# Kernel tuning notes

Hardware: AMD Instinct MI355X
Metric: run time of the kernel (lower is better)

## Reference

```python
import jax, jax.numpy as jnp
import numpy as np

B, T, D, H = 2, 2048, 1024, 16
HD = D // H  # head_dim = 64


def apply_rope(x, cos, sin):
    # x: [B, H, T, HD]; cos/sin: [1, 1, T, HD//2]
    x1, x2 = x[..., ::2], x[..., 1::2]
    y1 = x1 * cos - x2 * sin
    y2 = x1 * sin + x2 * cos
    # interleave back: [..., HD//2, 2] -> [..., HD]
    return jnp.stack([y1, y2], axis=-1).reshape(x.shape)


def setup_inputs() -> dict:
    key = jax.random.key(0)
    ks = jax.random.split(key, 11)
    s = 0.02
    return {
        "x": jax.random.normal(ks[0], (B, T, D), jnp.float32),
        "cos": jax.random.normal(ks[1], (1, 1, T, HD // 2), jnp.float32),
        "sin": jax.random.normal(ks[2], (1, 1, T, HD // 2), jnp.float32),
        "Wq": jax.random.normal(ks[3], (D, D), jnp.float32) * s,
        "bq": jax.random.normal(ks[4], (D,), jnp.float32) * s,
        "Wk": jax.random.normal(ks[5], (D, D), jnp.float32) * s,
        "bk": jax.random.normal(ks[6], (D,), jnp.float32) * s,
        "Wv": jax.random.normal(ks[7], (D, D), jnp.float32) * s,
        "bv": jax.random.normal(ks[8], (D,), jnp.float32) * s,
        "Wo": jax.random.normal(ks[9], (D, D), jnp.float32) * s,
        "bo": jax.random.normal(ks[10], (D,), jnp.float32) * s,
    }


def reference(x, cos, sin, Wq, bq, Wk, bk, Wv, bv, Wo, bo):
    b, t, d = x.shape
    # projections (nn.Linear: x @ W.T + b)
    q = (x @ Wq.T + bq).reshape(b, t, H, HD).transpose(0, 2, 1, 3)
    k = (x @ Wk.T + bk).reshape(b, t, H, HD).transpose(0, 2, 1, 3)
    v = (x @ Wv.T + bv).reshape(b, t, H, HD).transpose(0, 2, 1, 3)
    q = apply_rope(q, cos, sin)
    k = apply_rope(k, cos, sin)
    scores = jnp.einsum("bhqd,bhkd->bhqk", q, k) / jnp.sqrt(jnp.asarray(HD, x.dtype))
    # causal mask: query i attends to keys j <= i
    causal = jnp.tril(jnp.ones((t, t), dtype=bool))
    scores = jnp.where(causal, scores, jnp.asarray(-jnp.inf, x.dtype))
    weights = jax.nn.softmax(scores, axis=-1)
    out = jnp.einsum("bhqk,bhkd->bhqd", weights, v)
    out = out.transpose(0, 2, 1, 3).reshape(b, t, d)
    return out @ Wo.T + bo
```

## Files before the change

kernel.cpp:

```cpp
#include <hip/hip_runtime.h>
#include <hip/hip_bf16.h>
#include <cstdint>
#include <cstddef>

typedef __attribute__((ext_vector_type(8))) short bf16x8;
typedef __attribute__((ext_vector_type(4))) float f32x4;
typedef __attribute__((ext_vector_type(16))) float f32x16;

#define SCALE2 0.180336880111112f
#define VSTRIDE 2080

__device__ __forceinline__ unsigned short f2bf(float f) {
    unsigned u = __builtin_bit_cast(unsigned, f);
    unsigned r = (u + 0x7FFFu + ((u >> 16) & 1u)) >> 16;
    return (unsigned short)r;
}

__device__ __forceinline__ void gload16(const unsigned short* g, unsigned short* l) {
    __builtin_amdgcn_global_load_lds(
        (const __attribute__((address_space(1))) unsigned int*)(g),
        (__attribute__((address_space(3))) unsigned int*)(l), 16, 0, 0);
}

__global__ void cvt_all(const float* __restrict__ x,
                        const float* __restrict__ wq, const float* __restrict__ wk,
                        const float* __restrict__ wv, const float* __restrict__ wo,
                        unsigned short* __restrict__ xb,
                        unsigned short* __restrict__ wqb, unsigned short* __restrict__ wkb,
                        unsigned short* __restrict__ wvb, unsigned short* __restrict__ wob)
{
    const int y = blockIdx.y;
    const float* src; unsigned short* dst; int n;
    switch (y) {
        case 0: src = x;  dst = xb;  n = 4194304; break;
        case 1: src = wq; dst = wqb; n = 1048576; break;
        case 2: src = wk; dst = wkb; n = 1048576; break;
        case 3: src = wv; dst = wvb; n = 1048576; break;
        default: src = wo; dst = wob; n = 1048576; break;
    }
    const int i = (blockIdx.x * 256 + threadIdx.x) * 4;
    if (i < n) {
        float4 v = *(const float4*)(src + i);
        ushort4 o;
        o.x = f2bf(v.x); o.y = f2bf(v.y); o.z = f2bf(v.z); o.w = f2bf(v.w);
        *(ushort4*)(dst + i) = o;
    }
}

__global__ __launch_bounds__(256) void gemm_qkv(
    const unsigned short* __restrict__ xb,
    const unsigned short* __restrict__ wqb,
    const unsigned short* __restrict__ wkb,
    const unsigned short* __restrict__ wvb,
    const float* __restrict__ bq, const float* __restrict__ bk, const float* __restrict__ bv,
    const float* __restrict__ cosT, const float* __restrict__ sinT,
    unsigned short* __restrict__ Qb, unsigned short* __restrict__ Kb, unsigned short* __restrict__ Vtg)
{
    const int z = blockIdx.z;
    const unsigned short* wb = (z == 0) ? wqb : ((z == 1) ? wkb : wvb);
    const float* bias = (z == 0) ? bq : ((z == 1) ? bk : bv);
    unsigned short* dst = (z == 0) ? Qb : Kb;

    __shared__ __align__(16) unsigned short Al[128 * 32];
    __shared__ __align__(16) unsigned short Bl[128 * 32];
    __shared__ __align__(16) unsigned short Ct[128 * 136];

    const int tid = threadIdx.x;
    const int lane = tid & 63;
    const int w = tid >> 6;
    const int wr = w >> 1, wc = w & 1;
    const int lr = lane & 15, lg = lane >> 4;
    const int m0 = blockIdx.y * 128;
    const int n0 = blockIdx.x * 128;
    const int srow = tid >> 2, sseg = tid & 3;
    const int wbase = tid & 192;

    f32x4 acc[4][4] = {};

    for (int k0 = 0; k0 < 1024; k0 += 32) {
        __syncthreads();
#pragma unroll
        for (int p = 0; p < 2; ++p) {
            const int row = srow + p * 64;
            gload16(xb + (size_t)(m0 + row) * 1024 + k0 + sseg * 8, Al + (p * 256 + wbase) * 8);
            gload16(wb + (size_t)(n0 + row) * 1024 + k0 + sseg * 8, Bl + (p * 256 + wbase) * 8);
        }
        __syncthreads();
        bf16x8 af[4], bfr[4];
#pragma unroll
        for (int mt = 0; mt < 4; ++mt)
            af[mt] = *(const bf16x8*)(Al + (wr * 64 + mt * 16 + lr) * 32 + lg * 8);
#pragma unroll
        for (int nt = 0; nt < 4; ++nt)
            bfr[nt] = *(const bf16x8*)(Bl + (wc * 64 + nt * 16 + lr) * 32 + lg * 8);
#pragma unroll
        for (int mt = 0; mt < 4; ++mt)
#pragma unroll
            for (int nt = 0; nt < 4; ++nt)
                acc[mt][nt] = __builtin_amdgcn_mfma_f32_16x16x32_bf16(af[mt], bfr[nt], acc[mt][nt], 0, 0, 0);
    }

#pragma unroll
    for (int mt = 0; mt < 4; ++mt) {
#pragma unroll
        for (int nt = 0; nt < 4; ++nt) {
            const int coln = wc * 64 + nt * 16 + lr;
            const int col = n0 + coln;
            const float bcol = bias[col];
            const int hd = col & 63;
#pragma unroll
            for (int r = 0; r < 4; ++r) {
                const int rowm = wr * 64 + mt * 16 + lg * 4 + r;
                float v = acc[mt][nt][r] + bcol;
                if (z < 2) {
                    float part = __shfl_xor(v, 1);
                    const int tt = (m0 + rowm) & 2047;
                    const int i = hd >> 1;
                    const float cc = cosT[tt * 32 + i], ss = sinT[tt * 32 + i];
                    v = (hd & 1) ? (part * ss + v * cc) : (v * cc - part * ss);
                    if (z == 0) v *= SCALE2;
                    Ct[rowm * 136 + coln] = f2bf(v);
                } else {
                    Ct[coln * 136 + rowm] = f2bf(v);
                }
            }
        }
    }
    __syncthreads();
    if (z < 2) {
#pragma unroll
        for (int p = 0; p < 8; ++p) {
            const int u = p * 256 + tid;
            const int row = u >> 4, seg = u & 15;
            bf16x8 vv = *(const bf16x8*)(Ct + row * 136 + seg * 8);
            const int mrow = m0 + row;
            const int tt = mrow & 2047, bb = mrow >> 11;
            const int col = n0 + seg * 8;
            const int h = col >> 6, hd = col & 63;
            *(bf16x8*)(dst + ((size_t)(bb * 16 + h) * 2048 + tt) * 64 + hd) = vv;
        }
    } else {
        const int bb = m0 >> 11;
#pragma unroll
        for (int p = 0; p < 8; ++p) {
            const int u = p * 256 + tid;
            const int vrow = u >> 4, seg = u & 15;
            bf16x8 vv = *(const bf16x8*)(Ct + vrow * 136 + seg * 8);
            const int col = n0 + vrow;
            const int h = col >> 6, hd = col & 63;
            const int tt = (m0 + seg * 8) & 2047;
            *(bf16x8*)(Vtg + ((size_t)(bb * 16 + h) * 64 + hd) * VSTRIDE + tt) = vv;
        }
    }
}

__global__ __launch_bounds__(256, 2) void attn_fwd(
    const unsigned short* __restrict__ Qb, const unsigned short* __restrict__ Kb,
    const unsigned short* __restrict__ Vtg, unsigned short* __restrict__ attnb)
{
    __shared__ __align__(16) unsigned short Kl[2][32 * 64];
    __shared__ __align__(16) unsigned short Vl[2][64 * 32];
    __shared__ __align__(16) float Om[2][32][64];
    __shared__ float Ms[2][64];

    const int tid = threadIdx.x, lane = tid & 63, w = tid >> 6;
    const int l31 = lane & 31, lh = lane >> 5;
    const int bid = blockIdx.x;
    const int bh = bid & 31;
    const int pi = bid >> 5;
    const int half = w >> 1;
    const int slice = w & 1;
    const int cH = 63 - pi;
    const int c = half ? pi : cH;
    const size_t base = (size_t)bh * 131072;
    const int myq = c * 32 + l31;

    const unsigned short* Kg = Kb + base;
    const unsigned short* Vg = Vtg + (size_t)bh * (64 * VSTRIDE);

    bf16x8 qf[4];
#pragma unroll
    for (int s = 0; s < 4; ++s)
        qf[s] = *(const bf16x8*)(Qb + base + (size_t)myq * 64 + s * 16 + lh * 8);

    f32x16 o0 = {}, o1 = {};
    float sm = 0.f;

    const int krow = tid >> 3, kseg = (tid & 7) ^ (krow & 7);
    const int vrow = tid >> 2, vseg = (tid & 3) ^ (vrow & 3);
    const int ldst = (tid & ~63) * 8;

#define STAGE(T, B)                                                                  \
    {                                                                                \
        gload16(Kg + (size_t)((T) * 32 + krow) * 64 + kseg * 8, &Kl[B][ldst]);       \
        gload16(Vg + (size_t)vrow * VSTRIDE + (T) * 32 + vseg * 8, &Vl[B][ldst]);    \
    }

    STAGE(0, 0);
    for (int t = 0; t <= cH; ++t) {
        asm volatile("s_waitcnt vmcnt(0)" ::: "memory");
        __syncthreads();
        if (t + 1 <= cH) STAGE(t + 1, (t + 1) & 1);
        if (t <= c && (t & 1) == slice) {
            const unsigned short* Kc = Kl[t & 1];
            const unsigned short* Vc = Vl[t & 1];
            const int kvb = t * 32;

            bf16x8 kf0 = *(const bf16x8*)(Kc + l31 * 64 + (((0 * 2 + lh)) ^ (l31 & 7)) * 8);
            bf16x8 kf1 = *(const bf16x8*)(Kc + l31 * 64 + (((1 * 2 + lh)) ^ (l31 & 7)) * 8);
            bf16x8 kf2 = *(const bf16x8*)(Kc + l31 * 64 + (((2 * 2 + lh)) ^ (l31 & 7)) * 8);
            bf16x8 kf3 = *(const bf16x8*)(Kc + l31 * 64 + (((3 * 2 + lh)) ^ (l31 & 7)) * 8);

            f32x16 st = {};
            st = __builtin_amdgcn_mfma_f32_32x32x16_bf16(kf0, qf[0], st, 0, 0, 0);
            st = __builtin_amdgcn_mfma_f32_32x32x16_bf16(kf1, qf[1], st, 0, 0, 0);
            st = __builtin_amdgcn_mfma_f32_32x32x16_bf16(kf2, qf[2], st, 0, 0, 0);
            st = __builtin_amdgcn_mfma_f32_32x32x16_bf16(kf3, qf[3], st, 0, 0, 0);

            if (t == c) {
#pragma unroll
                for (int r = 0; r < 16; ++r) {
                    const int kv = kvb + (r & 3) + 8 * (r >> 2) + 4 * lh;
                    st[r] = (kv <= myq) ? st[r] : -1e30f;
                }
            }
#pragma unroll
            for (int r = 0; r < 16; ++r) st[r] = exp2f(st[r]);
            {
                float a0 = st[0] + st[1], a1 = st[2] + st[3];
                float a2 = st[4] + st[5], a3 = st[6] + st[7];
                float a4 = st[8] + st[9], a5 = st[10] + st[11];
                float a6 = st[12] + st[13], a7 = st[14] + st[15];
                sm += ((a0 + a1) + (a2 + a3)) + ((a4 + a5) + (a6 + a7));
            }

            unsigned pw0, pw1, pw2, pw3, pw4, pw5, pw6, pw7;
            {
                unsigned a0, a1, b0, b1;
                asm("v_cvt_pk_bf16_f32 %0, %1, %2" : "=v"(a0) : "v"(st[0]), "v"(st[1]));
                asm("v_cvt_pk_bf16_f32 %0, %1, %2" : "=v"(a1) : "v"(st[2]), "v"(st[3]));
                asm("v_cvt_pk_bf16_f32 %0, %1, %2" : "=v"(b0) : "v"(st[4]), "v"(st[5]));
                asm("v_cvt_pk_bf16_f32 %0, %1, %2" : "=v"(b1) : "v"(st[6]), "v"(st[7]));
                asm("v_permlane32_swap_b32 %0, %1" : "+v"(a0), "+v"(b0));
                asm("v_permlane32_swap_b32 %0, %1" : "+v"(a1), "+v"(b1));
                pw0 = a0; pw1 = a1; pw2 = b0; pw3 = b1;
            }
            {
                unsigned a0, a1, b0, b1;
                asm("v_cvt_pk_bf16_f32 %0, %1, %2" : "=v"(a0) : "v"(st[8]), "v"(st[9]));
                asm("v_cvt_pk_bf16_f32 %0, %1, %2" : "=v"(a1) : "v"(st[10]), "v"(st[11]));
                asm("v_cvt_pk_bf16_f32 %0, %1, %2" : "=v"(b0) : "v"(st[12]), "v"(st[13]));
                asm("v_cvt_pk_bf16_f32 %0, %1, %2" : "=v"(b1) : "v"(st[14]), "v"(st[15]));
                asm("v_permlane32_swap_b32 %0, %1" : "+v"(a0), "+v"(b0));
                asm("v_permlane32_swap_b32 %0, %1" : "+v"(a1), "+v"(b1));
                pw4 = a0; pw5 = a1; pw6 = b0; pw7 = b1;
            }

            const int vsw = l31 & 3;
            bf16x8 vf00 = *(const bf16x8*)(Vc + l31 * 32 + ((lh) ^ vsw) * 8);
            bf16x8 vf01 = *(const bf16x8*)(Vc + l31 * 32 + ((2 + lh) ^ vsw) * 8);
            bf16x8 vf10 = *(const bf16x8*)(Vc + (32 + l31) * 32 + ((lh) ^ vsw) * 8);
            bf16x8 vf11 = *(const bf16x8*)(Vc + (32 + l31) * 32 + ((2 + lh) ^ vsw) * 8);

            uint4 h0 = make_uint4(pw0, pw1, pw2, pw3);
            uint4 h1 = make_uint4(pw4, pw5, pw6, pw7);
            bf16x8 pf0 = __builtin_bit_cast(bf16x8, h0);
            bf16x8 pf1 = __builtin_bit_cast(bf16x8, h1);
            o0 = __builtin_amdgcn_mfma_f32_32x32x16_bf16(vf00, pf0, o0, 0, 0, 0);
            o1 = __builtin_amdgcn_mfma_f32_32x32x16_bf16(vf10, pf0, o1, 0, 0, 0);
            o0 = __builtin_amdgcn_mfma_f32_32x32x16_bf16(vf01, pf1, o0, 0, 0, 0);
            o1 = __builtin_amdgcn_mfma_f32_32x32x16_bf16(vf11, pf1, o1, 0, 0, 0);
        }
    }

    sm += __shfl_xor(sm, 32);

    __syncthreads();
    if (slice == 1) {
#pragma unroll
        for (int i = 0; i < 16; ++i) Om[half][i][lane] = o0[i];
#pragma unroll
        for (int i = 0; i < 16; ++i) Om[half][16 + i][lane] = o1[i];
        Ms[half][lane] = sm;
    }
    __syncthreads();
    if (slice == 0) {
        const float s = sm + Ms[half][lane];
        const float inv = 1.f / s;
        const int b = bh >> 4, h = bh & 15;
        unsigned short* obase = attnb + ((size_t)(b * 2048 + myq)) * 1024 + h * 64;
#pragma unroll
        for (int g = 0; g < 4; ++g) {
            ushort4 u;
            u.x = f2bf((o0[g * 4 + 0] + Om[half][g * 4 + 0][lane]) * inv);
            u.y = f2bf((o0[g * 4 + 1] + Om[half][g * 4 + 1][lane]) * inv);
            u.z = f2bf((o0[g * 4 + 2] + Om[half][g * 4 + 2][lane]) * inv);
            u.w = f2bf((o0[g * 4 + 3] + Om[half][g * 4 + 3][lane]) * inv);
            *(ushort4*)(obase + g * 8 + lh * 4) = u;
            ushort4 v;
            v.x = f2bf((o1[g * 4 + 0] + Om[half][16 + g * 4 + 0][lane]) * inv);
            v.y = f2bf((o1[g * 4 + 1] + Om[half][16 + g * 4 + 1][lane]) * inv);
            v.z = f2bf((o1[g * 4 + 2] + Om[half][16 + g * 4 + 2][lane]) * inv);
            v.w = f2bf((o1[g * 4 + 3] + Om[half][16 + g * 4 + 3][lane]) * inv);
            *(ushort4*)(obase + 32 + g * 8 + lh * 4) = v;
        }
    }
#undef STAGE
}

__global__ __launch_bounds__(256) void gemm_out(
    const unsigned short* __restrict__ ab,
    const unsigned short* __restrict__ wob,
    const float* __restrict__ bo,
    float* __restrict__ out)
{
    __shared__ __align__(16) unsigned short Al[128 * 32];
    __shared__ __align__(16) unsigned short Bl[64 * 32];

    const int tid = threadIdx.x;
    const int lane = tid & 63;
    const int w = tid >> 6;
    const int lr = lane & 15, lg = lane >> 4;
    const int m0 = blockIdx.y * 128;
    const int n0 = blockIdx.x * 64;

    f32x4 acc[2][4] = {};

    for (int k0 = 0; k0 < 1024; k0 += 32) {
        __syncthreads();
#pragma unroll
        for (int p = 0; p < 2; ++p) {
            const int u = p * 256 + tid;
            const int row = u >> 2, seg = u & 3;
            gload16(ab + (size_t)(m0 + row) * 1024 + k0 + seg * 8, Al + (u & ~63) * 8);
        }
        {
            const int u = tid;
            const int row = u >> 2, seg = u & 3;
            gload16(wob + (size_t)(n0 + row) * 1024 + k0 + seg * 8, Bl + (u & ~63) * 8);
        }
        __syncthreads();
        bf16x8 af[2], bfr[4];
#pragma unroll
        for (int mt = 0; mt < 2; ++mt)
            af[mt] = *(const bf16x8*)(Al + (w * 32 + mt * 16 + lr) * 32 + lg * 8);
#pragma unroll
        for (int nt = 0; nt < 4; ++nt)
            bfr[nt] = *(const bf16x8*)(Bl + (nt * 16 + lr) * 32 + lg * 8);
#pragma unroll
        for (int mt = 0; mt < 2; ++mt)
#pragma unroll
            for (int nt = 0; nt < 4; ++nt)
                acc[mt][nt] = __builtin_amdgcn_mfma_f32_16x16x32_bf16(af[mt], bfr[nt], acc[mt][nt], 0, 0, 0);
    }

#pragma unroll
    for (int mt = 0; mt < 2; ++mt) {
#pragma unroll
        for (int nt = 0; nt < 4; ++nt) {
            const int col = n0 + nt * 16 + lr;
            const float bcol = bo[col];
#pragma unroll
            for (int r = 0; r < 4; ++r) {
                const int mrow = m0 + w * 32 + mt * 16 + lg * 4 + r;
                out[(size_t)mrow * 1024 + col] = acc[mt][nt][r] + bcol;
            }
        }
    }
}

extern "C" void kernel_launch(void* const* d_in, const int* in_sizes, int n_in,
                              void* d_out, int out_size, void* d_ws, size_t ws_size,
                              hipStream_t stream) {
    const float* x    = (const float*)d_in[0];
    const float* cosT = (const float*)d_in[1];
    const float* sinT = (const float*)d_in[2];
    const float* Wq   = (const float*)d_in[3];
    const float* bq   = (const float*)d_in[4];
    const float* Wk   = (const float*)d_in[5];
    const float* bk   = (const float*)d_in[6];
    const float* Wv   = (const float*)d_in[7];
    const float* bv   = (const float*)d_in[8];
    const float* Wo   = (const float*)d_in[9];
    const float* bo   = (const float*)d_in[10];
    float* out = (float*)d_out;

    char* ws = (char*)d_ws;
    unsigned short* xb    = (unsigned short*)(ws + 0);
    unsigned short* attnb = (unsigned short*)(ws + 0);
    unsigned short* wob   = (unsigned short*)(ws + 8388608);
    unsigned short* wqb   = (unsigned short*)(ws + 10485760);
    unsigned short* wkb   = (unsigned short*)(ws + 12582912);
    unsigned short* wvb   = (unsigned short*)(ws + 14680064);
    unsigned short* Qb    = (unsigned short*)(ws + 16777216);
    unsigned short* Kb    = (unsigned short*)(ws + 25165824);
    unsigned short* Vtg   = (unsigned short*)(ws + 33554432);

    cvt_all<<<dim3(4096, 5), 256, 0, stream>>>(x, Wq, Wk, Wv, Wo, xb, wqb, wkb, wvb, wob);
    gemm_qkv<<<dim3(8, 32, 3), 256, 0, stream>>>(xb, wqb, wkb, wvb, bq, bk, bv,
                                                 cosT, sinT, Qb, Kb, Vtg);
    attn_fwd<<<dim3(1024), 256, 0, stream>>>(Qb, Kb, Vtg, attnb);
    gemm_out<<<dim3(16, 32), 256, 0, stream>>>(attnb, wob, bo, out);
}
```

Measured before the change: 131.6 us.

## Triple-buffer attention K/V loads and remap GEMM blocks for XCD-local L2 reuse

The attention kernel moves from double to triple buffering of K/V tiles in one shared byte buffer. It prefetches two tiles ahead and waits with vmcnt(2), so global loads overlap compute longer. The shared region is reused for the final cross-warp reduction. Both GEMMs switch to a 1D grid whose block index maps tiles so that blocks on the same XCD (bid&7) share A/B row and column panels, aiming at better L2 locality. The trade-off is more LDS per attention block, which may lower occupancy, and more index arithmetic.

```diff
diff --git a/kernel.cpp b/kernel.cpp
--- a/kernel.cpp
+++ b/kernel.cpp
@@ -56,7 +56,15 @@
     const float* __restrict__ cosT, const float* __restrict__ sinT,
     unsigned short* __restrict__ Qb, unsigned short* __restrict__ Kb, unsigned short* __restrict__ Vtg)
 {
-    const int z = blockIdx.z;
+    const int bid = blockIdx.x;
+    const int xcd = bid & 7;
+    const int s = bid >> 3;
+    const int i4 = xcd >> 1, k2 = xcd & 1;
+    const int z = s >> 5;
+    const int tt = s & 31;
+    const int m0 = (i4 * 8 + (tt >> 2)) * 128;
+    const int n0 = (k2 * 4 + (tt & 3)) * 128;
+
     const unsigned short* wb = (z == 0) ? wqb : ((z == 1) ? wkb : wvb);
     const float* bias = (z == 0) ? bq : ((z == 1) ? bk : bv);
     unsigned short* dst = (z == 0) ? Qb : Kb;
@@ -70,8 +78,6 @@
     const int w = tid >> 6;
     const int wr = w >> 1, wc = w & 1;
     const int lr = lane & 15, lg = lane >> 4;
-    const int m0 = blockIdx.y * 128;
-    const int n0 = blockIdx.x * 128;
     const int srow = tid >> 2, sseg = tid & 3;
     const int wbase = tid & 192;
 
@@ -114,9 +120,9 @@
                 float v = acc[mt][nt][r] + bcol;
                 if (z < 2) {
                     float part = __shfl_xor(v, 1);
-                    const int tt = (m0 + rowm) & 2047;
+                    const int ttm = (m0 + rowm) & 2047;
                     const int i = hd >> 1;
-                    const float cc = cosT[tt * 32 + i], ss = sinT[tt * 32 + i];
+                    const float cc = cosT[ttm * 32 + i], ss = sinT[ttm * 32 + i];
                     v = (hd & 1) ? (part * ss + v * cc) : (v * cc - part * ss);
                     if (z == 0) v *= SCALE2;
                     Ct[rowm * 136 + coln] = f2bf(v);
@@ -134,10 +140,10 @@
             const int row = u >> 4, seg = u & 15;
             bf16x8 vv = *(const bf16x8*)(Ct + row * 136 + seg * 8);
             const int mrow = m0 + row;
-            const int tt = mrow & 2047, bb = mrow >> 11;
+            const int ttm = mrow & 2047, bb = mrow >> 11;
             const int col = n0 + seg * 8;
             const int h = col >> 6, hd = col & 63;
-            *(bf16x8*)(dst + ((size_t)(bb * 16 + h) * 2048 + tt) * 64 + hd) = vv;
+            *(bf16x8*)(dst + ((size_t)(bb * 16 + h) * 2048 + ttm) * 64 + hd) = vv;
         }
     } else {
         const int bb = m0 >> 11;
@@ -148,8 +154,8 @@
             bf16x8 vv = *(const bf16x8*)(Ct + vrow * 136 + seg * 8);
             const int col = n0 + vrow;
             const int h = col >> 6, hd = col & 63;
-            const int tt = (m0 + seg * 8) & 2047;
-            *(bf16x8*)(Vtg + ((size_t)(bb * 16 + h) * 64 + hd) * VSTRIDE + tt) = vv;
+            const int ttm = (m0 + seg * 8) & 2047;
+            *(bf16x8*)(Vtg + ((size_t)(bb * 16 + h) * 64 + hd) * VSTRIDE + ttm) = vv;
         }
     }
 }
@@ -158,10 +164,7 @@
     const unsigned short* __restrict__ Qb, const unsigned short* __restrict__ Kb,
     const unsigned short* __restrict__ Vtg, unsigned short* __restrict__ attnb)
 {
-    __shared__ __align__(16) unsigned short Kl[2][32 * 64];
-    __shared__ __align__(16) unsigned short Vl[2][64 * 32];
-    __shared__ __align__(16) float Om[2][32][64];
-    __shared__ float Ms[2][64];
+    __shared__ __align__(16) unsigned char smem[25088];
 
     const int tid = threadIdx.x, lane = tid & 63, w = tid >> 6;
     const int l31 = lane & 31, lh = lane >> 5;
@@ -190,26 +193,37 @@
     const int vrow = tid >> 2, vseg = (tid & 3) ^ (vrow & 3);
     const int ldst = (tid & ~63) * 8;
 
-#define STAGE(T, B)                                                                  \
-    {                                                                                \
-        gload16(Kg + (size_t)((T) * 32 + krow) * 64 + kseg * 8, &Kl[B][ldst]);       \
-        gload16(Vg + (size_t)vrow * VSTRIDE + (T) * 32 + vseg * 8, &Vl[B][ldst]);    \
+#define STAGE(T, B)                                                                   \
+    {                                                                                 \
+        unsigned short* kb_ = (unsigned short*)(smem + (B) * 8192);                   \
+        unsigned short* vb_ = (unsigned short*)(smem + (B) * 8192 + 4096);            \
+        gload16(Kg + (size_t)((T) * 32 + krow) * 64 + kseg * 8, kb_ + ldst);          \
+        gload16(Vg + (size_t)vrow * VSTRIDE + (T) * 32 + vseg * 8, vb_ + ldst);       \
     }
 
     STAGE(0, 0);
+    STAGE(1, 1);
+    int bsel = 0;
     for (int t = 0; t <= cH; ++t) {
-        asm volatile("s_waitcnt vmcnt(0)" ::: "memory");
+        if (t < cH) asm volatile("s_waitcnt vmcnt(2)" ::: "memory");
+        else        asm volatile("s_waitcnt vmcnt(0)" ::: "memory");
         __syncthreads();
-        if (t + 1 <= cH) STAGE(t + 1, (t + 1) & 1);
+        {
+            const int t2 = t + 2;
+            if (t2 <= cH) {
+                int b2 = bsel + 2; if (b2 >= 3) b2 -= 3;
+                STAGE(t2, b2);
+            }
+        }
         if (t <= c && (t & 1) == slice) {
-            const unsigned short* Kc = Kl[t & 1];
-            const unsigned short* Vc = Vl[t & 1];
+            const unsigned short* Kc = (const unsigned short*)(smem + bsel * 8192);
+            const unsigned short* Vc = Kc + 2048;
             const int kvb = t * 32;
 
-            bf16x8 kf0 = *(const bf16x8*)(Kc + l31 * 64 + (((0 * 2 + lh)) ^ (l31 & 7)) * 8);
-            bf16x8 kf1 = *(const bf16x8*)(Kc + l31 * 64 + (((1 * 2 + lh)) ^ (l31 & 7)) * 8);
-            bf16x8 kf2 = *(const bf16x8*)(Kc + l31 * 64 + (((2 * 2 + lh)) ^ (l31 & 7)) * 8);
-            bf16x8 kf3 = *(const bf16x8*)(Kc + l31 * 64 + (((3 * 2 + lh)) ^ (l31 & 7)) * 8);
+            bf16x8 kf0 = *(const bf16x8*)(Kc + l31 * 64 + ((0 * 2 + lh) ^ (l31 & 7)) * 8);
+            bf16x8 kf1 = *(const bf16x8*)(Kc + l31 * 64 + ((1 * 2 + lh) ^ (l31 & 7)) * 8);
+            bf16x8 kf2 = *(const bf16x8*)(Kc + l31 * 64 + ((2 * 2 + lh) ^ (l31 & 7)) * 8);
+            bf16x8 kf3 = *(const bf16x8*)(Kc + l31 * 64 + ((3 * 2 + lh) ^ (l31 & 7)) * 8);
 
             f32x16 st = {};
             st = __builtin_amdgcn_mfma_f32_32x32x16_bf16(kf0, qf[0], st, 0, 0, 0);
@@ -271,37 +285,40 @@
             o0 = __builtin_amdgcn_mfma_f32_32x32x16_bf16(vf01, pf1, o0, 0, 0, 0);
             o1 = __builtin_amdgcn_mfma_f32_32x32x16_bf16(vf11, pf1, o1, 0, 0, 0);
         }
+        bsel += 1; if (bsel == 3) bsel = 0;
     }
 
     sm += __shfl_xor(sm, 32);
 
+    float* Om = (float*)smem;
+    float* Ms = (float*)(smem + 16384);
     __syncthreads();
     if (slice == 1) {
 #pragma unroll
-        for (int i = 0; i < 16; ++i) Om[half][i][lane] = o0[i];
-#pragma unroll
-        for (int i = 0; i < 16; ++i) Om[half][16 + i][lane] = o1[i];
-        Ms[half][lane] = sm;
+        for (int i = 0; i < 16; ++i) Om[(half * 32 + i) * 64 + lane] = o0[i];
+#pragma unroll
+        for (int i = 0; i < 16; ++i) Om[(half * 32 + 16 + i) * 64 + lane] = o1[i];
+        Ms[half * 64 + lane] = sm;
     }
     __syncthreads();
     if (slice == 0) {
-        const float s = sm + Ms[half][lane];
+        const float s = sm + Ms[half * 64 + lane];
         const float inv = 1.f / s;
         const int b = bh >> 4, h = bh & 15;
         unsigned short* obase = attnb + ((size_t)(b * 2048 + myq)) * 1024 + h * 64;
 #pragma unroll
         for (int g = 0; g < 4; ++g) {
             ushort4 u;
-            u.x = f2bf((o0[g * 4 + 0] + Om[half][g * 4 + 0][lane]) * inv);
-            u.y = f2bf((o0[g * 4 + 1] + Om[half][g * 4 + 1][lane]) * inv);
-            u.z = f2bf((o0[g * 4 + 2] + Om[half][g * 4 + 2][lane]) * inv);
-            u.w = f2bf((o0[g * 4 + 3] + Om[half][g * 4 + 3][lane]) * inv);
+            u.x = f2bf((o0[g * 4 + 0] + Om[(half * 32 + g * 4 + 0) * 64 + lane]) * inv);
+            u.y = f2bf((o0[g * 4 + 1] + Om[(half * 32 + g * 4 + 1) * 64 + lane]) * inv);
+            u.z = f2bf((o0[g * 4 + 2] + Om[(half * 32 + g * 4 + 2) * 64 + lane]) * inv);
+            u.w = f2bf((o0[g * 4 + 3] + Om[(half * 32 + g * 4 + 3) * 64 + lane]) * inv);
             *(ushort4*)(obase + g * 8 + lh * 4) = u;
             ushort4 v;
-            v.x = f2bf((o1[g * 4 + 0] + Om[half][16 + g * 4 + 0][lane]) * inv);
-            v.y = f2bf((o1[g * 4 + 1] + Om[half][16 + g * 4 + 1][lane]) * inv);
-            v.z = f2bf((o1[g * 4 + 2] + Om[half][16 + g * 4 + 2][lane]) * inv);
-            v.w = f2bf((o1[g * 4 + 3] + Om[half][16 + g * 4 + 3][lane]) * inv);
+            v.x = f2bf((o1[g * 4 + 0] + Om[(half * 32 + 16 + g * 4 + 0) * 64 + lane]) * inv);
+            v.y = f2bf((o1[g * 4 + 1] + Om[(half * 32 + 16 + g * 4 + 1) * 64 + lane]) * inv);
+            v.z = f2bf((o1[g * 4 + 2] + Om[(half * 32 + 16 + g * 4 + 2) * 64 + lane]) * inv);
+            v.w = f2bf((o1[g * 4 + 3] + Om[(half * 32 + 16 + g * 4 + 3) * 64 + lane]) * inv);
             *(ushort4*)(obase + 32 + g * 8 + lh * 4) = v;
         }
     }
@@ -317,12 +334,17 @@
     __shared__ __align__(16) unsigned short Al[128 * 32];
     __shared__ __align__(16) unsigned short Bl[64 * 32];
 
+    const int bid = blockIdx.x;
+    const int xcd = bid & 7;
+    const int s = bid >> 3;
+    const int i4 = xcd >> 1, k2 = xcd & 1;
+    const int m0 = (i4 * 8 + (s >> 3)) * 128;
+    const int n0 = (k2 * 8 + (s & 7)) * 64;
+
     const int tid = threadIdx.x;
     const int lane = tid & 63;
     const int w = tid >> 6;
     const int lr = lane & 15, lg = lane >> 4;
-    const int m0 = blockIdx.y * 128;
-    const int n0 = blockIdx.x * 64;
 
     f32x4 acc[2][4] = {};
 
@@ -397,8 +419,8 @@
     unsigned short* Vtg   = (unsigned short*)(ws + 33554432);
 
     cvt_all<<<dim3(4096, 5), 256, 0, stream>>>(x, Wq, Wk, Wv, Wo, xb, wqb, wkb, wvb, wob);
-    gemm_qkv<<<dim3(8, 32, 3), 256, 0, stream>>>(xb, wqb, wkb, wvb, bq, bk, bv,
-                                                 cosT, sinT, Qb, Kb, Vtg);
+    gemm_qkv<<<dim3(768), 256, 0, stream>>>(xb, wqb, wkb, wvb, bq, bk, bv,
+                                            cosT, sinT, Qb, Kb, Vtg);
     attn_fwd<<<dim3(1024), 256, 0, stream>>>(Qb, Kb, Vtg, attnb);
-    gemm_out<<<dim3(16, 32), 256, 0, stream>>>(attnb, wob, bo, out);
-}
+    gemm_out<<<dim3(512), 256, 0, stream>>>(attnb, wob, bo, out);
+}
```

After: 119.1 us. -9.5%, faster.
